# Kernel optimization log

Hardware: AMD Instinct MI355X
Metric: run time of the kernel (lower is better)

## Reference

```python
import jax, jax.numpy as jnp
import numpy as np
from jax import lax

B, N, D = 4, 4096, 1024
H, DH, K = 8, 128, 256  # heads, dim_head, linformer k
KERNEL = 32
PAD = (15, 16)  # torch padding='same' for even kernel: left=(k-1)//2, right=rest


def setup_inputs() -> dict:
    key = jax.random.key(0)
    ks = jax.random.split(key, 7)
    s = 0.02
    return {
        "x": jax.random.normal(ks[0], (B, N, D), dtype=jnp.float32),
        "Wq": jax.random.normal(ks[1], (D, D), dtype=jnp.float32) * s,
        "Wk": jax.random.normal(ks[2], (D, D), dtype=jnp.float32) * s,
        "Wpk": jax.random.normal(ks[3], (K, N, KERNEL), dtype=jnp.float32) * s,
        "bpk": jax.random.normal(ks[4], (K,), dtype=jnp.float32) * s,
        "Wo": jax.random.normal(ks[5], (D, D), dtype=jnp.float32) * s,
        "bo": jax.random.normal(ks[6], (D,), dtype=jnp.float32) * s,
    }


def reference(x, Wq, Wk, Wpk, bpk, Wo, bo):
    b, n, d = x.shape
    # linear projections (torch Linear: y = x @ W.T)
    q = x @ Wq.T                       # (b, n, h*dh)
    keys = x @ Wk.T                    # (b, n, h*dh)
    # Conv1d over feature length with seq positions as channels: (b, n, d) -> (b, k, d)
    keys = lax.conv_general_dilated(
        keys, Wpk, window_strides=(1,), padding=[PAD],
        dimension_numbers=("NCH", "OIH", "NCH"),
    ) + bpk[None, :, None]             # (b, K, h*dh)
    values = keys                      # share_kv=True
    # split heads
    q = q.reshape(b, n, H, DH).transpose(0, 2, 1, 3)        # (b, h, n, dh)
    kk = keys.reshape(b, K, H, DH).transpose(0, 2, 1, 3)    # (b, h, K, dh)
    vv = values.reshape(b, K, H, DH).transpose(0, 2, 1, 3)  # (b, h, K, dh)
    dots = jnp.einsum("bhnd,bhkd->bhnk", q, kk) * (DH ** -0.5)
    attn = jax.nn.softmax(dots, axis=-1)                    # dropout p=0.0 (eval)
    out = jnp.einsum("bhnk,bhkd->bhnd", attn, vv)
    out = out.transpose(0, 2, 1, 3).reshape(b, n, H * DH)
    return out @ Wo.T + bo
```

## Files before the change

### kernel.cpp

```cpp
#include <hip/hip_runtime.h>


typedef short v8s __attribute__((ext_vector_type(8)));
typedef float v4f __attribute__((ext_vector_type(4)));

#define MFMA16(a, b, c) __builtin_amdgcn_mfma_f32_16x16x32_bf16((a), (b), (c), 0, 0, 0)
#define WAITV(N) asm volatile("s_waitcnt vmcnt(" #N ")" ::: "memory")
#define SBAR() __builtin_amdgcn_s_barrier()

__device__ __forceinline__ unsigned short f2bf(float f) {
  unsigned int u = __float_as_uint(f);
  u += 0x7fffu + ((u >> 16) & 1u);
  return (unsigned short)(u >> 16);
}

__device__ __forceinline__ v8s cvt8(float4 a, float4 b) {
  v8s v;
  v[0] = (short)f2bf(a.x); v[1] = (short)f2bf(a.y);
  v[2] = (short)f2bf(a.z); v[3] = (short)f2bf(a.w);
  v[4] = (short)f2bf(b.x); v[5] = (short)f2bf(b.y);
  v[6] = (short)f2bf(b.z); v[7] = (short)f2bf(b.w);
  return v;
}

__device__ __forceinline__ void gld16(void* lds, const void* g) {
  __builtin_amdgcn_global_load_lds(
      (const __attribute__((address_space(1))) void*)g,
      (__attribute__((address_space(3))) void*)lds, 16, 0, 0);
}

__device__ __forceinline__ const v8s* frag_ptr(const short* base, int row, int g) {
  return (const v8s*)(base + row * 32 + (((g ^ (row >> 1)) & 3) << 3));
}

__global__ __launch_bounds__(256) void k_cvt(const float* __restrict__ src,
                                             short* __restrict__ dst, int n8) {
  const int i = blockIdx.x * 256 + threadIdx.x;
  if (i >= n8) return;
  const float4* s = (const float4*)src;
  ((v8s*)dst)[i] = cvt8(s[2 * i], s[2 * i + 1]);
}

__global__ __launch_bounds__(256) void k_reorder_wpk(const float* __restrict__ Wpk,
                                                     short* __restrict__ Wr) {
  __shared__ short T[64][40];
  const int k  = blockIdx.x >> 6;
  const int n0 = (blockIdx.x & 63) << 6;
  const int tid = threadIdx.x;
  {
    const int i = tid >> 2, t0 = (tid & 3) << 3;
    const float* p = Wpk + ((size_t)k * 4096 + n0 + i) * 32 + t0;
    float4 a = *(const float4*)p, b = *(const float4*)(p + 4);
    *(v8s*)&T[i][t0] = cvt8(a, b);
  }
  __syncthreads();
  {
    const int t = tid >> 3, j0 = (tid & 7) << 3;
    v8s o;
#pragma unroll
    for (int q = 0; q < 8; ++q) o[q] = T[j0 + q][t];
    *(v8s*)(Wr + ((size_t)t * 256 + k) * 4096 + n0 + j0) = o;
  }
}

__global__ __launch_bounds__(256) void k_zero_pad(short* __restrict__ KpTp) {
  const int idx = blockIdx.x * 256 + threadIdx.x;
  const int ridx = idx >> 9, col8 = idx & 511;
  const int b = ridx >> 5, rr = ridx & 31;
  const int row = (rr < 15) ? rr : 1039 + (rr - 15);
  v8s z = {0, 0, 0, 0, 0, 0, 0, 0};
  *(v8s*)(KpTp + ((size_t)b * 1056 + row) * 4096 + col8 * 8) = z;
}

__global__ __launch_bounds__(256) void k_gemm_qk_v3(const short* __restrict__ xbf,
                                                    const short* __restrict__ Wqk,
                                                    short* __restrict__ Qbf,
                                                    short* __restrict__ Kp) {
  __shared__ short As[2][128][32];
  __shared__ short Bs[2][128][32];
  const int tid = threadIdx.x, lane = tid & 63, w = tid >> 6;
  const int m0 = blockIdx.x * 128, j0 = blockIdx.y * 128;
  const int wr = (w >> 1) * 64, wc = (w & 1) * 64;
  const int l15 = lane & 15, g = lane >> 4;
  const int sr = lane >> 2, sseg = lane & 3;

  v4f acc[4][4];
#pragma unroll
  for (int i = 0; i < 4; ++i)
#pragma unroll
    for (int j = 0; j < 4; ++j) acc[i][j] = (v4f)0.0f;

  auto stage = [&](int buf, int k0) {
#pragma unroll
    for (int q0 = 0; q0 < 2; ++q0) {
      const int rblk = (w * 2 + q0) << 4, r = rblk + sr;
      const int co = ((sseg ^ (r >> 1)) & 3) << 3;
      gld16(&As[buf][rblk][0], xbf + (size_t)(m0 + r) * 1024 + k0 + co);
      gld16(&Bs[buf][rblk][0], Wqk + (size_t)(j0 + r) * 1024 + k0 + co);
    }
  };

  stage(0, 0);
#pragma unroll 1
  for (int p = 0, buf = 0; p < 32; ++p, buf ^= 1) {
    if (p + 1 < 32) stage(buf ^ 1, (p + 1) * 32);
    if (p < 31) { WAITV(4); } else { WAITV(0); }
    SBAR();
    v8s af[4], bf4[4];
#pragma unroll
    for (int mi = 0; mi < 4; ++mi)
      af[mi] = *frag_ptr(&As[buf][0][0], wr + mi * 16 + l15, g);
#pragma unroll
    for (int ni = 0; ni < 4; ++ni)
      bf4[ni] = *frag_ptr(&Bs[buf][0][0], wc + ni * 16 + l15, g);
#pragma unroll
    for (int ni = 0; ni < 4; ++ni)
#pragma unroll
      for (int mi = 0; mi < 4; ++mi)
        acc[mi][ni] = MFMA16(af[mi], bf4[ni], acc[mi][ni]);
    SBAR();
  }
  const int rbase = (lane >> 4) * 4;
#pragma unroll
  for (int mi = 0; mi < 4; ++mi)
#pragma unroll
    for (int ni = 0; ni < 4; ++ni) {
      const int col = j0 + wc + ni * 16 + l15;
      short* dst = (col < 1024) ? Qbf : Kp;
      const int cj = (col < 1024) ? col : col - 1024;
#pragma unroll
      for (int r = 0; r < 4; ++r) {
        const int row = m0 + wr + mi * 16 + rbase + r;
        dst[(size_t)row * 1024 + cj] = (short)f2bf(acc[mi][ni][r]);
      }
    }
}

__global__ __launch_bounds__(256) void k_transpose_pad(const short* __restrict__ src,
                                                       short* __restrict__ dst) {
  __shared__ short T[64][72];
  const int r0 = blockIdx.x * 64, c0 = blockIdx.y * 64, b = blockIdx.z;
  const int tid = threadIdx.x;
  {
    const int i = tid >> 2, q = (tid & 3) << 4;
    const short* ps = src + ((size_t)b * 4096 + r0 + i) * 1024 + c0 + q;
    *(v8s*)&T[i][q]     = *(const v8s*)ps;
    *(v8s*)&T[i][q + 8] = *(const v8s*)(ps + 8);
  }
  __syncthreads();
  {
    const int j = tid >> 2, p = (tid & 3) << 4;
    v8s o0, o1;
#pragma unroll
    for (int t = 0; t < 8; ++t) o0[t] = T[p + t][j];
#pragma unroll
    for (int t = 0; t < 8; ++t) o1[t] = T[p + 8 + t][j];
    short* pd = dst + ((size_t)b * 1056 + 15 + c0 + j) * 4096 + r0 + p;
    *(v8s*)pd = o0;
    *(v8s*)(pd + 8) = o1;
  }
}

__global__ __launch_bounds__(512, 4) void k_conv_v5(const short* __restrict__ Wr,
                                                    const short* __restrict__ KpTp,
                                                    float* __restrict__ Pq) {
  __shared__ short A[3][256][32];
  __shared__ short Kt[2][160][32];
  const int bid = blockIdx.x;
  const int ns = (bid & 7) | (((bid >> 8) & 1) << 3);
  const int j  = (bid >> 3) & 31;
  const int b = j >> 3, nt = j & 7;
  const int D0 = nt * 128;
  const int nbase = ns * 256;
  const int tid = threadIdx.x, lane = tid & 63, w = tid >> 6;
  const int wm = (w >> 1) * 64, wn = (w & 1) * 64;
  const int l15 = lane & 15, g = lane >> 4;
  const int lr = lane >> 2, lseg = lane & 3;
  const short* KpTb = KpTp + (size_t)b * 1056 * 4096;

  v4f acc[4][4];
#pragma unroll
  for (int mi = 0; mi < 4; ++mi)
#pragma unroll
    for (int ni = 0; ni < 4; ++ni) acc[mi][ni] = (v4f)0.0f;

  auto stageA = [&](int buf, int s2, int q) {
    const int t2 = s2 & 31, c2 = s2 >> 5;
    const int rblk = q * 128 + w * 16;
    const int row = rblk + lr;
    const int sg = ((lseg ^ (row >> 1)) & 3) << 3;
    gld16(&A[buf][rblk][0],
          Wr + ((size_t)t2 * 256 + row) * 4096 + nbase + c2 * 32 + sg);
  };
  auto stageKt = [&](int buf, int c1, int q) {
    const int rblk = q * 128 + w * 16;
    const int row = rblk + lr;
    const int srow = row < 159 ? row : 158;
    const int sg = ((lseg ^ (row >> 1)) & 3) << 3;
    gld16(&Kt[buf][rblk][0],
          KpTb + (size_t)(D0 + srow) * 4096 + nbase + c1 * 32 + sg);
  };

  stageA(0, 0, 0); stageA(0, 0, 1);
  stageKt(0, 0, 0);
  if (w < 2) stageKt(0, 0, 1);
  stageA(1, 1, 0); stageA(1, 1, 1);
  WAITV(2);
  SBAR();

  int ab = 0, pab = 2;
#pragma unroll 1
  for (int s = 0; s < 256; ++s) {
    const int t = s & 31, c = s >> 5;
    const short* Abp = &A[ab][0][0];
    const short* Ktp = &Kt[c & 1][0][0];
    v8s aq[4], bq[4];
#pragma unroll
    for (int mi = 0; mi < 4; ++mi)
      aq[mi] = *frag_ptr(Abp, wm + mi * 16 + l15, g);
#pragma unroll
    for (int ni = 0; ni < 4; ++ni)
      bq[ni] = *frag_ptr(Ktp, wn + ni * 16 + l15 + t, g);
    if (s + 2 < 256) { stageA(pab, s + 2, 0); stageA(pab, s + 2, 1); }
    const bool kt0 = (t == 26) && (c < 7);
    const bool kt1 = (t == 27) && (c < 7);
    if (kt0) stageKt((c + 1) & 1, c + 1, 0);
    if (kt1 && w < 2) stageKt((c + 1) & 1, c + 1, 1);
    __builtin_amdgcn_s_setprio(1);
#pragma unroll
    for (int ni = 0; ni < 4; ++ni)
#pragma unroll
      for (int mi = 0; mi < 4; ++mi)
        acc[mi][ni] = MFMA16(aq[mi], bq[ni], acc[mi][ni]);
    __builtin_amdgcn_s_setprio(0);
    if (s < 254) {
      if (kt0 || kt1) { WAITV(3); } else { WAITV(2); }
    } else if (s == 254) {
      WAITV(0);
    }
    SBAR();
    pab = ab; ab = (ab == 2) ? 0 : ab + 1;
  }

  float* Pp = Pq + (size_t)(ns * 4 + b) * 262144;
#pragma unroll
  for (int mi = 0; mi < 4; ++mi)
#pragma unroll
    for (int ni = 0; ni < 4; ++ni) {
      const int col = D0 + wn + ni * 16 + l15;
#pragma unroll
      for (int r = 0; r < 4; ++r)
        Pp[(size_t)(wm + mi * 16 + g * 4 + r) * 1024 + col] = acc[mi][ni][r];
    }
}

__global__ __launch_bounds__(256) void k_reduce_kc(const float* __restrict__ P,
                                                   const float* __restrict__ bpk,
                                                   float* __restrict__ Kc) {
  const int i = (blockIdx.x * 256 + threadIdx.x) * 4;
  const float bias = bpk[(i >> 10) & 255];
  float4 s; s.x = bias; s.y = bias; s.z = bias; s.w = bias;
#pragma unroll
  for (int ns = 0; ns < 16; ++ns) {
    float4 v = *(const float4*)(P + (size_t)ns * 1048576 + i);
    s.x += v.x; s.y += v.y; s.z += v.z; s.w += v.w;
  }
  *(float4*)(Kc + i) = s;
}

__global__ __launch_bounds__(256) void k_kc_post(const float* __restrict__ Kc,
                                                 short* __restrict__ Kcbf,
                                                 short* __restrict__ KcT) {
  __shared__ short T[64][72];
  const int k0 = blockIdx.x * 64, d0 = blockIdx.y * 64, b = blockIdx.z;
  const int tid = threadIdx.x;
  {
    const int i = tid >> 2, q = (tid & 3) << 4;
    const float* ps = Kc + (size_t)(b * 256 + k0 + i) * 1024 + d0 + q;
    float4 f0 = *(const float4*)ps,       f1 = *(const float4*)(ps + 4);
    float4 f2 = *(const float4*)(ps + 8), f3 = *(const float4*)(ps + 12);
    v8s v0 = cvt8(f0, f1), v1 = cvt8(f2, f3);
    *(v8s*)&T[i][q] = v0;
    *(v8s*)&T[i][q + 8] = v1;
    short* pc = Kcbf + (size_t)(b * 256 + k0 + i) * 1024 + d0 + q;
    *(v8s*)pc = v0;
    *(v8s*)(pc + 8) = v1;
  }
  __syncthreads();
  {
    const int j = tid >> 2, p = (tid & 3) << 4;
    v8s o0, o1;
#pragma unroll
    for (int t = 0; t < 8; ++t) o0[t] = T[p + t][j];
#pragma unroll
    for (int t = 0; t < 8; ++t) o1[t] = T[p + 8 + t][j];
    short* pd = KcT + (size_t)(b * 1024 + d0 + j) * 256 + k0 + p;
    *(v8s*)pd = o0;
    *(v8s*)(pd + 8) = o1;
  }
}

__global__ __launch_bounds__(256) void k_attn(const short* __restrict__ Qbf,
                                              const short* __restrict__ Kcbf,
                                              const short* __restrict__ KcT,
                                              short* __restrict__ AO) {
  __shared__ short P[4][16][264];
  const int nt = blockIdx.x, h = blockIdx.y, b = blockIdx.z;
  const int tid = threadIdx.x, lane = tid & 63, w = tid >> 6;
  const int l15 = lane & 15, lg4 = (lane >> 4) * 4, lg8 = (lane >> 4) * 8;
  const float scale = 0.08838834764831845f;
  const size_t qb  = (size_t)b * 4096 * 1024 + (size_t)h * 128;
  const size_t kb  = (size_t)b * 256 * 1024 + (size_t)h * 128;
  const size_t vtb = ((size_t)b * 1024 + (size_t)h * 128) * 256;
  short (*Pw)[264] = P[w];
  const int n_wave = nt * 128 + w * 32;

#pragma unroll 1
  for (int half = 0; half < 2; ++half) {
    const int nbase = n_wave + half * 16;
    v8s aq[4];
#pragma unroll
    for (int kt = 0; kt < 4; ++kt)
      aq[kt] = *(const v8s*)(Qbf + qb + (size_t)(nbase + l15) * 1024 + kt * 32 + lg8);

    v4f dacc[16];
#pragma unroll
    for (int ct = 0; ct < 16; ++ct) dacc[ct] = (v4f)0.0f;
#pragma unroll 1
    for (int kt = 0; kt < 4; ++kt) {
#pragma unroll
      for (int ct = 0; ct < 16; ++ct) {
        v8s bk = *(const v8s*)(Kcbf + kb + (size_t)(ct * 16 + l15) * 1024 + kt * 32 + lg8);
        dacc[ct] = MFMA16(aq[kt], bk, dacc[ct]);
      }
    }
#pragma unroll
    for (int ct = 0; ct < 16; ++ct) dacc[ct] = dacc[ct] * scale;
    v4f m4 = dacc[0];
#pragma unroll
    for (int ct = 1; ct < 16; ++ct)
#pragma unroll
      for (int r = 0; r < 4; ++r) m4[r] = fmaxf(m4[r], dacc[ct][r]);
#pragma unroll
    for (int off = 1; off < 16; off <<= 1)
#pragma unroll
      for (int r = 0; r < 4; ++r) m4[r] = fmaxf(m4[r], __shfl_xor(m4[r], off, 64));
    v4f ssum = (v4f)0.0f;
#pragma unroll
    for (int ct = 0; ct < 16; ++ct)
#pragma unroll
      for (int r = 0; r < 4; ++r) {
        const float e = __expf(dacc[ct][r] - m4[r]);
        ssum[r] += e;
        Pw[lg4 + r][ct * 16 + l15] = (short)f2bf(e);
      }
#pragma unroll
    for (int off = 1; off < 16; off <<= 1)
#pragma unroll
      for (int r = 0; r < 4; ++r) ssum[r] += __shfl_xor(ssum[r], off, 64);
    __syncthreads();

    v4f oacc[8];
#pragma unroll
    for (int ct = 0; ct < 8; ++ct) oacc[ct] = (v4f)0.0f;
#pragma unroll 1
    for (int kt2 = 0; kt2 < 8; ++kt2) {
      v8s pa = *(const v8s*)&Pw[l15][kt2 * 32 + lg8];
#pragma unroll
      for (int ct = 0; ct < 8; ++ct) {
        v8s bv = *(const v8s*)(KcT + vtb + (size_t)(ct * 16 + l15) * 256 + kt2 * 32 + lg8);
        oacc[ct] = MFMA16(pa, bv, oacc[ct]);
      }
    }
    v4f inv;
#pragma unroll
    for (int r = 0; r < 4; ++r) inv[r] = 1.0f / ssum[r];
#pragma unroll
    for (int ct = 0; ct < 8; ++ct)
#pragma unroll
      for (int r = 0; r < 4; ++r)
        AO[qb + (size_t)(nbase + lg4 + r) * 1024 + ct * 16 + l15] =
            (short)f2bf(oacc[ct][r] * inv[r]);
    __syncthreads();
  }
}

__global__ __launch_bounds__(256) void k_gemm_out_v3(const short* __restrict__ AO,
                                                     const short* __restrict__ Wobf,
                                                     const float* __restrict__ bo,
                                                     float* __restrict__ out) {
  __shared__ short As[2][128][32];
  __shared__ short Bs[2][128][32];
  const int tid = threadIdx.x, lane = tid & 63, w = tid >> 6;
  const int m0 = blockIdx.x * 128, j0 = blockIdx.y * 128;
  const int wr = (w >> 1) * 64, wc = (w & 1) * 64;
  const int l15 = lane & 15, g = lane >> 4;
  const int sr = lane >> 2, sseg = lane & 3;

  v4f acc[4][4];
#pragma unroll
  for (int i = 0; i < 4; ++i)
#pragma unroll
    for (int j = 0; j < 4; ++j) acc[i][j] = (v4f)0.0f;

  auto stage = [&](int buf, int k0) {
#pragma unroll
    for (int q0 = 0; q0 < 2; ++q0) {
      const int rblk = (w * 2 + q0) << 4, r = rblk + sr;
      const int co = ((sseg ^ (r >> 1)) & 3) << 3;
      gld16(&As[buf][rblk][0], AO + (size_t)(m0 + r) * 1024 + k0 + co);
      gld16(&Bs[buf][rblk][0], Wobf + (size_t)(j0 + r) * 1024 + k0 + co);
    }
  };

  stage(0, 0);
#pragma unroll 1
  for (int p = 0, buf = 0; p < 32; ++p, buf ^= 1) {
    if (p + 1 < 32) stage(buf ^ 1, (p + 1) * 32);
    if (p < 31) { WAITV(4); } else { WAITV(0); }
    SBAR();
    v8s af[4], bf4[4];
#pragma unroll
    for (int mi = 0; mi < 4; ++mi)
      af[mi] = *frag_ptr(&As[buf][0][0], wr + mi * 16 + l15, g);
#pragma unroll
    for (int ni = 0; ni < 4; ++ni)
      bf4[ni] = *frag_ptr(&Bs[buf][0][0], wc + ni * 16 + l15, g);
#pragma unroll
    for (int ni = 0; ni < 4; ++ni)
#pragma unroll
      for (int mi = 0; mi < 4; ++mi)
        acc[mi][ni] = MFMA16(af[mi], bf4[ni], acc[mi][ni]);
    SBAR();
  }
  const int rbase = (lane >> 4) * 4;
#pragma unroll
  for (int mi = 0; mi < 4; ++mi)
#pragma unroll
    for (int ni = 0; ni < 4; ++ni) {
      const int col = j0 + wc + ni * 16 + l15;
      const float bias = bo[col];
#pragma unroll
      for (int r = 0; r < 4; ++r) {
        const int row = m0 + wr + mi * 16 + rbase + r;
        out[(size_t)row * 1024 + col] = acc[mi][ni][r] + bias;
      }
    }
}

extern "C" void kernel_launch(void* const* d_in, const int* in_sizes, int n_in,
                              void* d_out, int out_size, void* d_ws, size_t ws_size,
                              hipStream_t stream) {
  const float* x   = (const float*)d_in[0];
  const float* Wq  = (const float*)d_in[1];
  const float* Wk  = (const float*)d_in[2];
  const float* Wpk = (const float*)d_in[3];
  const float* bpk = (const float*)d_in[4];
  const float* Wo  = (const float*)d_in[5];
  const float* bo  = (const float*)d_in[6];

  const size_t OFF_WR   = 0;
  const size_t OFF_XBF  = 67108864;
  const size_t OFF_WQK  = 100663296;
  const size_t OFF_KPTP = 67108864;
  const size_t OFF_KCBF = 67108864;
  const size_t OFF_KCT  = 69206016;
  const size_t OFF_WOBF = 101711872;
  const size_t OFF_QBF  = 104857600;
  const size_t OFF_KP   = 138412032;
  const size_t OFF_KC   = 171966464;
  const size_t NEED     = 176160768;
  if (ws_size < NEED) return;

  char* ws = (char*)d_ws;
  short* Wr   = (short*)(ws + OFF_WR);
  short* xbf  = (short*)(ws + OFF_XBF);
  short* Wqk  = (short*)(ws + OFF_WQK);
  short* KpTp = (short*)(ws + OFF_KPTP);
  short* Kcbf = (short*)(ws + OFF_KCBF);
  short* KcT  = (short*)(ws + OFF_KCT);
  short* Wobf = (short*)(ws + OFF_WOBF);
  short* Qbf  = (short*)(ws + OFF_QBF);
  short* Kp   = (short*)(ws + OFF_KP);
  float* Kc   = (float*)(ws + OFF_KC);
  short* AO   = Kp;
  float* Ppart = (float*)d_out;
  float* outp = (float*)d_out;

  k_cvt<<<dim3(8192), dim3(256), 0, stream>>>(x, xbf, 16777216 / 8);
  k_cvt<<<dim3(512),  dim3(256), 0, stream>>>(Wq, Wqk, 1048576 / 8);
  k_cvt<<<dim3(512),  dim3(256), 0, stream>>>(Wk, Wqk + 1048576, 1048576 / 8);
  k_reorder_wpk<<<dim3(16384), dim3(256), 0, stream>>>(Wpk, Wr);
  k_gemm_qk_v3<<<dim3(128, 16), dim3(256), 0, stream>>>(xbf, Wqk, Qbf, Kp);
  k_transpose_pad<<<dim3(64, 16, 4), dim3(256), 0, stream>>>(Kp, KpTp);
  k_cvt<<<dim3(512), dim3(256), 0, stream>>>(Wo, Wobf, 1048576 / 8);
  k_zero_pad<<<dim3(256), dim3(256), 0, stream>>>(KpTp);
  k_conv_v5<<<dim3(512), dim3(512), 0, stream>>>(Wr, KpTp, Ppart);
  k_reduce_kc<<<dim3(1024), dim3(256), 0, stream>>>(Ppart, bpk, Kc);
  k_kc_post<<<dim3(4, 16, 4), dim3(256), 0, stream>>>(Kc, Kcbf, KcT);
  k_attn<<<dim3(32, 8, 4), dim3(256), 0, stream>>>(Qbf, Kcbf, KcT, AO);
  k_gemm_out_v3<<<dim3(128, 8), dim3(256), 0, stream>>>(AO, Wobf, bo, outp);
}
```

Baseline: 608.3 us.

## Enlarge per-wave tiles to 64x128 in QK GEMM and conv kernels

In both the QK projection GEMM and the conv GEMM, each wave now computes a 64x128 output tile (4x8 MFMA fragments) instead of 64x64. The QK GEMM block tile grows to 256x128, and the conv kernel drops from 512 to 256 threads per block. Each A fragment read from LDS is now reused across twice as many B fragments, which cuts LDS reads per MFMA. The cost is a doubled accumulator register footprint, which may lower occupancy, and each thread issues more staging loads, with waitcnt values adjusted to match.

```diff
diff --git a/kernel.cpp b/kernel.cpp
--- a/kernel.cpp
+++ b/kernel.cpp
@@ -72,30 +72,35 @@
   *(v8s*)(KpTp + ((size_t)b * 1056 + row) * 4096 + col8 * 8) = z;
 }
 
-__global__ __launch_bounds__(256) void k_gemm_qk_v3(const short* __restrict__ xbf,
-                                                    const short* __restrict__ Wqk,
-                                                    short* __restrict__ Qbf,
-                                                    short* __restrict__ Kp) {
-  __shared__ short As[2][128][32];
+__global__ __launch_bounds__(256, 2) void k_gemm_qk_v4(const short* __restrict__ xbf,
+                                                       const short* __restrict__ Wqk,
+                                                       short* __restrict__ Qbf,
+                                                       short* __restrict__ Kp) {
+  __shared__ short As[2][256][32];
   __shared__ short Bs[2][128][32];
   const int tid = threadIdx.x, lane = tid & 63, w = tid >> 6;
-  const int m0 = blockIdx.x * 128, j0 = blockIdx.y * 128;
-  const int wr = (w >> 1) * 64, wc = (w & 1) * 64;
+  const int m0 = blockIdx.x * 256, j0 = blockIdx.y * 128;
+  const int wm = w * 64;
   const int l15 = lane & 15, g = lane >> 4;
-  const int sr = lane >> 2, sseg = lane & 3;
-
-  v4f acc[4][4];
+  const int lr = lane >> 2, lseg = lane & 3;
+
+  v4f acc[4][8];
 #pragma unroll
   for (int i = 0; i < 4; ++i)
 #pragma unroll
-    for (int j = 0; j < 4; ++j) acc[i][j] = (v4f)0.0f;
+    for (int j = 0; j < 8; ++j) acc[i][j] = (v4f)0.0f;
 
   auto stage = [&](int buf, int k0) {
 #pragma unroll
-    for (int q0 = 0; q0 < 2; ++q0) {
-      const int rblk = (w * 2 + q0) << 4, r = rblk + sr;
-      const int co = ((sseg ^ (r >> 1)) & 3) << 3;
+    for (int q = 0; q < 4; ++q) {
+      const int rblk = q * 64 + w * 16, r = rblk + lr;
+      const int co = ((lseg ^ (r >> 1)) & 3) << 3;
       gld16(&As[buf][rblk][0], xbf + (size_t)(m0 + r) * 1024 + k0 + co);
+    }
+#pragma unroll
+    for (int q = 0; q < 2; ++q) {
+      const int rblk = q * 64 + w * 16, r = rblk + lr;
+      const int co = ((lseg ^ (r >> 1)) & 3) << 3;
       gld16(&Bs[buf][rblk][0], Wqk + (size_t)(j0 + r) * 1024 + k0 + co);
     }
   };
@@ -104,34 +109,40 @@
 #pragma unroll 1
   for (int p = 0, buf = 0; p < 32; ++p, buf ^= 1) {
     if (p + 1 < 32) stage(buf ^ 1, (p + 1) * 32);
-    if (p < 31) { WAITV(4); } else { WAITV(0); }
+    if (p < 31) { WAITV(6); } else { WAITV(0); }
     SBAR();
-    v8s af[4], bf4[4];
+    v8s af[4];
 #pragma unroll
     for (int mi = 0; mi < 4; ++mi)
-      af[mi] = *frag_ptr(&As[buf][0][0], wr + mi * 16 + l15, g);
-#pragma unroll
-    for (int ni = 0; ni < 4; ++ni)
-      bf4[ni] = *frag_ptr(&Bs[buf][0][0], wc + ni * 16 + l15, g);
-#pragma unroll
-    for (int ni = 0; ni < 4; ++ni)
-#pragma unroll
-      for (int mi = 0; mi < 4; ++mi)
-        acc[mi][ni] = MFMA16(af[mi], bf4[ni], acc[mi][ni]);
+      af[mi] = *frag_ptr(&As[buf][0][0], wm + mi * 16 + l15, g);
+    __builtin_amdgcn_s_setprio(1);
+#pragma unroll
+    for (int nh = 0; nh < 2; ++nh) {
+      v8s bq[4];
+#pragma unroll
+      for (int nj = 0; nj < 4; ++nj)
+        bq[nj] = *frag_ptr(&Bs[buf][0][0], nh * 64 + nj * 16 + l15, g);
+#pragma unroll
+      for (int nj = 0; nj < 4; ++nj)
+#pragma unroll
+        for (int mi = 0; mi < 4; ++mi)
+          acc[mi][nh * 4 + nj] = MFMA16(af[mi], bq[nj], acc[mi][nh * 4 + nj]);
+    }
+    __builtin_amdgcn_s_setprio(0);
     SBAR();
   }
-  const int rbase = (lane >> 4) * 4;
+  const int rbase = g * 4;
 #pragma unroll
   for (int mi = 0; mi < 4; ++mi)
 #pragma unroll
-    for (int ni = 0; ni < 4; ++ni) {
-      const int col = j0 + wc + ni * 16 + l15;
+    for (int nf = 0; nf < 8; ++nf) {
+      const int col = j0 + nf * 16 + l15;
       short* dst = (col < 1024) ? Qbf : Kp;
       const int cj = (col < 1024) ? col : col - 1024;
 #pragma unroll
       for (int r = 0; r < 4; ++r) {
-        const int row = m0 + wr + mi * 16 + rbase + r;
-        dst[(size_t)row * 1024 + cj] = (short)f2bf(acc[mi][ni][r]);
+        const int row = m0 + wm + mi * 16 + rbase + r;
+        dst[(size_t)row * 1024 + cj] = (short)f2bf(acc[mi][nf][r]);
       }
     }
 }
@@ -161,7 +172,7 @@
   }
 }
 
-__global__ __launch_bounds__(512, 4) void k_conv_v5(const short* __restrict__ Wr,
+__global__ __launch_bounds__(256, 2) void k_conv_v6(const short* __restrict__ Wr,
                                                     const short* __restrict__ KpTp,
                                                     float* __restrict__ Pq) {
   __shared__ short A[3][256][32];
@@ -173,84 +184,94 @@
   const int D0 = nt * 128;
   const int nbase = ns * 256;
   const int tid = threadIdx.x, lane = tid & 63, w = tid >> 6;
-  const int wm = (w >> 1) * 64, wn = (w & 1) * 64;
+  const int wm = w * 64;
   const int l15 = lane & 15, g = lane >> 4;
   const int lr = lane >> 2, lseg = lane & 3;
   const short* KpTb = KpTp + (size_t)b * 1056 * 4096;
 
-  v4f acc[4][4];
+  v4f acc[4][8];
 #pragma unroll
   for (int mi = 0; mi < 4; ++mi)
 #pragma unroll
-    for (int ni = 0; ni < 4; ++ni) acc[mi][ni] = (v4f)0.0f;
-
-  auto stageA = [&](int buf, int s2, int q) {
+    for (int ni = 0; ni < 8; ++ni) acc[mi][ni] = (v4f)0.0f;
+
+  auto stageA = [&](int buf, int s2) {
     const int t2 = s2 & 31, c2 = s2 >> 5;
-    const int rblk = q * 128 + w * 16;
-    const int row = rblk + lr;
-    const int sg = ((lseg ^ (row >> 1)) & 3) << 3;
-    gld16(&A[buf][rblk][0],
-          Wr + ((size_t)t2 * 256 + row) * 4096 + nbase + c2 * 32 + sg);
+#pragma unroll
+    for (int q = 0; q < 4; ++q) {
+      const int rblk = q * 64 + w * 16, row = rblk + lr;
+      const int sg = ((lseg ^ (row >> 1)) & 3) << 3;
+      gld16(&A[buf][rblk][0],
+            Wr + ((size_t)t2 * 256 + row) * 4096 + nbase + c2 * 32 + sg);
+    }
   };
-  auto stageKt = [&](int buf, int c1, int q) {
-    const int rblk = q * 128 + w * 16;
-    const int row = rblk + lr;
-    const int srow = row < 159 ? row : 158;
-    const int sg = ((lseg ^ (row >> 1)) & 3) << 3;
-    gld16(&Kt[buf][rblk][0],
-          KpTb + (size_t)(D0 + srow) * 4096 + nbase + c1 * 32 + sg);
+  auto stageKt = [&](int buf, int c1) {
+#pragma unroll
+    for (int q = 0; q < 2; ++q) {
+      const int rblk = q * 64 + w * 16, row = rblk + lr;
+      const int sg = ((lseg ^ (row >> 1)) & 3) << 3;
+      gld16(&Kt[buf][rblk][0],
+            KpTb + (size_t)(D0 + row) * 4096 + nbase + c1 * 32 + sg);
+    }
+    {
+      const int rblk = 128 + (w & 1) * 16, row = rblk + lr;
+      const int srow = row < 159 ? row : 158;
+      const int sg = ((lseg ^ (row >> 1)) & 3) << 3;
+      gld16(&Kt[buf][rblk][0],
+            KpTb + (size_t)(D0 + srow) * 4096 + nbase + c1 * 32 + sg);
+    }
   };
 
-  stageA(0, 0, 0); stageA(0, 0, 1);
-  stageKt(0, 0, 0);
-  if (w < 2) stageKt(0, 0, 1);
-  stageA(1, 1, 0); stageA(1, 1, 1);
-  WAITV(2);
+  stageA(0, 0);
+  stageKt(0, 0);
+  stageA(1, 1);
+  WAITV(4);
   SBAR();
 
-  int ab = 0, pab = 2;
 #pragma unroll 1
   for (int s = 0; s < 256; ++s) {
     const int t = s & 31, c = s >> 5;
+    const int ab = s % 3;
     const short* Abp = &A[ab][0][0];
     const short* Ktp = &Kt[c & 1][0][0];
-    v8s aq[4], bq[4];
+    const bool doKt = (t == 26) && (c < 7);
+    if (s + 2 < 256) stageA((s + 2) % 3, s + 2);
+    if (doKt) stageKt((c + 1) & 1, c + 1);
+    v8s af[4];
 #pragma unroll
     for (int mi = 0; mi < 4; ++mi)
-      aq[mi] = *frag_ptr(Abp, wm + mi * 16 + l15, g);
-#pragma unroll
-    for (int ni = 0; ni < 4; ++ni)
-      bq[ni] = *frag_ptr(Ktp, wn + ni * 16 + l15 + t, g);
-    if (s + 2 < 256) { stageA(pab, s + 2, 0); stageA(pab, s + 2, 1); }
-    const bool kt0 = (t == 26) && (c < 7);
-    const bool kt1 = (t == 27) && (c < 7);
-    if (kt0) stageKt((c + 1) & 1, c + 1, 0);
-    if (kt1 && w < 2) stageKt((c + 1) & 1, c + 1, 1);
+      af[mi] = *frag_ptr(Abp, wm + mi * 16 + l15, g);
     __builtin_amdgcn_s_setprio(1);
 #pragma unroll
-    for (int ni = 0; ni < 4; ++ni)
-#pragma unroll
-      for (int mi = 0; mi < 4; ++mi)
-        acc[mi][ni] = MFMA16(aq[mi], bq[ni], acc[mi][ni]);
+    for (int nh = 0; nh < 2; ++nh) {
+      v8s bq[4];
+#pragma unroll
+      for (int nj = 0; nj < 4; ++nj)
+        bq[nj] = *frag_ptr(Ktp, nh * 64 + nj * 16 + l15 + t, g);
+#pragma unroll
+      for (int nj = 0; nj < 4; ++nj)
+#pragma unroll
+        for (int mi = 0; mi < 4; ++mi)
+          acc[mi][nh * 4 + nj] = MFMA16(af[mi], bq[nj], acc[mi][nh * 4 + nj]);
+    }
     __builtin_amdgcn_s_setprio(0);
     if (s < 254) {
-      if (kt0 || kt1) { WAITV(3); } else { WAITV(2); }
+      if (doKt) { WAITV(7); } else { WAITV(4); }
     } else if (s == 254) {
       WAITV(0);
     }
     SBAR();
-    pab = ab; ab = (ab == 2) ? 0 : ab + 1;
   }
 
   float* Pp = Pq + (size_t)(ns * 4 + b) * 262144;
 #pragma unroll
   for (int mi = 0; mi < 4; ++mi)
 #pragma unroll
-    for (int ni = 0; ni < 4; ++ni) {
-      const int col = D0 + wn + ni * 16 + l15;
+    for (int nf = 0; nf < 8; ++nf) {
+      const int col = D0 + nf * 16 + l15;
 #pragma unroll
       for (int r = 0; r < 4; ++r)
-        Pp[(size_t)(wm + mi * 16 + g * 4 + r) * 1024 + col] = acc[mi][ni][r];
+        Pp[(size_t)(wm + mi * 16 + g * 4 + r) * 1024 + col] = acc[mi][nf][r];
     }
 }
 
@@ -491,11 +512,11 @@
   k_cvt<<<dim3(512),  dim3(256), 0, stream>>>(Wq, Wqk, 1048576 / 8);
   k_cvt<<<dim3(512),  dim3(256), 0, stream>>>(Wk, Wqk + 1048576, 1048576 / 8);
   k_reorder_wpk<<<dim3(16384), dim3(256), 0, stream>>>(Wpk, Wr);
-  k_gemm_qk_v3<<<dim3(128, 16), dim3(256), 0, stream>>>(xbf, Wqk, Qbf, Kp);
+  k_gemm_qk_v4<<<dim3(64, 16), dim3(256), 0, stream>>>(xbf, Wqk, Qbf, Kp);
   k_transpose_pad<<<dim3(64, 16, 4), dim3(256), 0, stream>>>(Kp, KpTp);
   k_cvt<<<dim3(512), dim3(256), 0, stream>>>(Wo, Wobf, 1048576 / 8);
   k_zero_pad<<<dim3(256), dim3(256), 0, stream>>>(KpTp);
-  k_conv_v5<<<dim3(512), dim3(512), 0, stream>>>(Wr, KpTp, Ppart);
+  k_conv_v6<<<dim3(512), dim3(256), 0, stream>>>(Wr, KpTp, Ppart);
   k_reduce_kc<<<dim3(1024), dim3(256), 0, stream>>>(Ppart, bpk, Kc);
   k_kc_post<<<dim3(4, 16, 4), dim3(256), 0, stream>>>(Kc, Kcbf, KcT);
   k_attn<<<dim3(32, 8, 4), dim3(256), 0, stream>>>(Qbf, Kcbf, KcT, AO);
```

After: 664.5 us. +9.2%, slower.
